# Kernel optimization log

Hardware: AMD Instinct MI355X
Metric: run time of the kernel (lower is better)

The kernel has to match this reference:

```python
import jax, jax.numpy as jnp
import numpy as np

BS, NQ, NTGT, NCLS, D = 16, 1024, 96, 4, 6
COST_CLASS, COST_BBOX = 1.0, 1.0
INF = jnp.float32(1e9)


def hungarian(cost):
    """Min-cost linear assignment (Jonker-Volgenant / e-maxx Hungarian).

    cost: (n, m) with n <= m. Returns (n,) int32: matched column for each row.
    Matches scipy.optimize.linear_sum_assignment's optimal assignment.
    """
    n, m = cost.shape
    # 1-indexed padded cost; row 0 / col 0 are virtual.
    a = jnp.zeros((n + 1, m + 1), jnp.float32).at[1:, 1:].set(cost.astype(jnp.float32))

    def assign_row(i, uvp):
        u, v, p = uvp  # p[j] = row matched to col j (0 = free)
        p = p.at[0].set(i)

        def dij_cond(c):
            _u, _v, _minv, _used, _way, j0 = c
            return p[j0] != 0

        def dij_body(c):
            u, v, minv, used, way, j0 = c
            used = used.at[j0].set(True)
            i0 = p[j0]
            cur = a[i0] - u[i0] - v                      # reduced costs, (m+1,)
            better = (cur < minv) & jnp.logical_not(used)
            minv = jnp.where(better, cur, minv)
            way = jnp.where(better, j0, way)
            masked = jnp.where(used, INF, minv)
            j1 = jnp.argmin(masked).astype(jnp.int32)
            delta = masked[j1]
            du = jnp.where(used, delta, jnp.float32(0))
            u = u.at[p].add(du)                          # u[p[j]] += delta for used j
            v = v - du
            minv = jnp.where(used, minv, minv - delta)
            return (u, v, minv, used, way, j1)

        minv0 = jnp.full(m + 1, INF, jnp.float32)
        used0 = jnp.zeros(m + 1, bool)
        way0 = jnp.zeros(m + 1, jnp.int32)
        u, v, _minv, _used, way, j0 = jax.lax.while_loop(
            dij_cond, dij_body, (u, v, minv0, used0, way0, jnp.int32(0)))

        def aug_cond(c):
            j0, _p = c
            return j0 != 0

        def aug_body(c):
            j0, p = c
            j1 = way[j0]
            p = p.at[j0].set(p[j1])
            return (j1, p)

        _, p = jax.lax.while_loop(aug_cond, aug_body, (j0, p))
        return (u, v, p)

    u0 = jnp.zeros(n + 1, jnp.float32)
    v0 = jnp.zeros(m + 1, jnp.float32)
    p0 = jnp.zeros(m + 1, jnp.int32)
    _, _, p = jax.lax.fori_loop(1, n + 1, assign_row, (u0, v0, p0))
    # invert: col4row[row] = col   (free cols / virtual col collapse into index 0)
    col4row = jnp.zeros(n + 1, jnp.int32).at[p[1:]].set(jnp.arange(1, m + 1, dtype=jnp.int32))
    return col4row[1:] - 1


def setup_inputs() -> dict:
    key = jax.random.key(0)
    k1, k2, k3, k4 = jax.random.split(key, 4)
    pred_logits = jax.random.normal(k1, (BS, NQ, NCLS), jnp.float32)
    pred_boxes = jax.random.uniform(k2, (BS, NQ, D), jnp.float32)
    labels = jax.random.randint(k3, (BS, NTGT), 0, NCLS, dtype=jnp.int32)
    control_points = jax.random.uniform(k4, (BS, NTGT, D), jnp.float32)
    return {"pred_logits": pred_logits, "pred_boxes": pred_boxes,
            "labels": labels, "control_points": control_points}


def reference(pred_logits, pred_boxes, labels, control_points):
    bs, nq, _ = pred_logits.shape
    ntgt = labels.shape[1]
    # cost matrix build (the memory-bound part)
    out_prob = jax.nn.softmax(pred_logits.reshape(bs * nq, -1), axis=-1)
    out_bbox = pred_boxes.reshape(bs * nq, -1)
    tgt_ids = labels.reshape(-1)
    tgt_bbox = control_points.reshape(bs * ntgt, -1)
    cost_class = -out_prob[:, tgt_ids]                              # (bs*nq, bs*ntgt)
    cost_bbox = jnp.abs(out_bbox[:, None, :] - tgt_bbox[None, :, :]).sum(-1)  # L1 cdist
    C = (COST_BBOX * cost_bbox + COST_CLASS * cost_class).reshape(bs, nq, bs * ntgt)

    # per-batch diagonal block -> Hungarian (targets as rows since ntgt <= nq)
    def per_batch(Cb, b):
        block = jax.lax.dynamic_slice(Cb, (0, b * ntgt), (nq, ntgt))  # (nq, ntgt)
        return hungarian(block.T)                                      # (ntgt,) matched query per target

    matched_query = jax.vmap(per_batch)(C, jnp.arange(bs, dtype=jnp.int32))
    return C, matched_query
```

## Files before the change

### kernel.cpp

```cpp
#include <hip/hip_runtime.h>


#define BSZ   16
#define NQ    1024
#define NTGT  96
#define NCLS  4
#define DD    6
#define NCOLS (BSZ * NTGT)
#define NROWS (BSZ * NQ)
#define LHINF 1e9f
#define NHB   16
#define ROWS_PER_BLK 8

typedef float f32x4 __attribute__((ext_vector_type(4)));

__device__ __forceinline__ float wave_fmin63(float x) {
    const int INF_I = __float_as_int(LHINF);
    int m;
    m = __builtin_amdgcn_update_dpp(INF_I, __float_as_int(x), 0x111, 0xf, 0xf, false);
    x = fminf(x, __int_as_float(m));
    m = __builtin_amdgcn_update_dpp(INF_I, __float_as_int(x), 0x112, 0xf, 0xf, false);
    x = fminf(x, __int_as_float(m));
    m = __builtin_amdgcn_update_dpp(INF_I, __float_as_int(x), 0x114, 0xf, 0xf, false);
    x = fminf(x, __int_as_float(m));
    m = __builtin_amdgcn_update_dpp(INF_I, __float_as_int(x), 0x118, 0xf, 0xf, false);
    x = fminf(x, __int_as_float(m));
    m = __builtin_amdgcn_update_dpp(INF_I, __float_as_int(x), 0x142, 0xf, 0xf, false);
    x = fminf(x, __int_as_float(m));
    m = __builtin_amdgcn_update_dpp(INF_I, __float_as_int(x), 0x143, 0xf, 0xf, false);
    x = fminf(x, __int_as_float(m));
    return x;
}

__device__ __forceinline__ float cost_elem6(const float* bx, const float* tv, float psel) {
    float cd = fabsf(bx[0] - tv[0]);
    cd += fabsf(bx[1] - tv[1]);
    cd += fabsf(bx[2] - tv[2]);
    cd += fabsf(bx[3] - tv[3]);
    cd += fabsf(bx[4] - tv[4]);
    cd += fabsf(bx[5] - tv[5]);
    return cd - psel;
}

__device__ __forceinline__ float4 softmax4(float4 lg) {
    const float mx = fmaxf(fmaxf(lg.x, lg.y), fmaxf(lg.z, lg.w));
    const float e0 = expf(lg.x - mx), e1 = expf(lg.y - mx);
    const float e2 = expf(lg.z - mx), e3 = expf(lg.w - mx);
    const float s = (e0 + e1) + (e2 + e3);
    return make_float4(e0 / s, e1 / s, e2 / s, e3 / s);
}

__global__ __launch_bounds__(256) void twsarg_kernel(
    const float* __restrict__ logits, const float* __restrict__ boxes,
    const int* __restrict__ labels, const float* __restrict__ tgt,
    float* __restrict__ tws, float* __restrict__ rowminv, int* __restrict__ rowarg)
{
    const int t = blockIdx.x;
    const int b = blockIdx.y;
    const int tr = b * NTGT + t;
    float tv[DD];
#pragma unroll
    for (int d = 0; d < DD; ++d) tv[d] = tgt[(size_t)tr * DD + d];
    const int cls = labels[tr];

    const int q4 = threadIdx.x * 4;
    const int row0 = b * NQ + q4;
    const float4* bx4 = (const float4*)(boxes + (size_t)row0 * DD);
    float bv[24];
#pragma unroll
    for (int c = 0; c < 6; ++c) {
        float4 f = bx4[c];
        bv[c * 4] = f.x; bv[c * 4 + 1] = f.y; bv[c * 4 + 2] = f.z; bv[c * 4 + 3] = f.w;
    }
    float o[4];
#pragma unroll
    for (int c = 0; c < 4; ++c) {
        const float4 p = softmax4(((const float4*)logits)[row0 + c]);
        const float ps = (cls == 0) ? p.x : (cls == 1) ? p.y : (cls == 2) ? p.z : p.w;
        o[c] = cost_elem6(bv + c * DD, tv, ps);
    }
    *((float4*)(tws + (size_t)tr * NQ + q4)) = make_float4(o[0], o[1], o[2], o[3]);

    float bvv = o[0]; int bj = q4;
    if (o[1] < bvv) { bvv = o[1]; bj = q4 + 1; }
    if (o[2] < bvv) { bvv = o[2]; bj = q4 + 2; }
    if (o[3] < bvv) { bvv = o[3]; bj = q4 + 3; }
#pragma unroll
    for (int off = 32; off > 0; off >>= 1) {
        const float ov = __shfl_down(bvv, off, 64);
        const int oj = __shfl_down(bj, off, 64);
        if (ov < bvv || (ov == bvv && oj < bj)) { bvv = ov; bj = oj; }
    }
    __shared__ float sv[4];
    __shared__ int sj[4];
    const int w = threadIdx.x >> 6;
    if ((threadIdx.x & 63) == 0) { sv[w] = bvv; sj[w] = bj; }
    __syncthreads();
    if (threadIdx.x == 0) {
        for (int i = 1; i < 4; ++i)
            if (sv[i] < bvv || (sv[i] == bvv && sj[i] < bj)) { bvv = sv[i]; bj = sj[i]; }
        rowminv[tr] = bvv; rowarg[tr] = bj;
    }
}

__global__ __launch_bounds__(384) void cost_kernel_fb(
    const float* __restrict__ logits, const float* __restrict__ boxes,
    const int* __restrict__ labels, const float* __restrict__ tgt,
    float* __restrict__ C)
{
    const int row = blockIdx.x;
    const int tid = threadIdx.x;
    const float4 pr = softmax4(*reinterpret_cast<const float4*>(logits + (size_t)row * NCLS));
    const float prr[4] = {pr.x, pr.y, pr.z, pr.w};
    float bx[DD];
#pragma unroll
    for (int d = 0; d < DD; ++d) bx[d] = boxes[(size_t)row * DD + d];
    const int colbase = tid * 4;
    const int4 lb = *reinterpret_cast<const int4*>(labels + colbase);
    const int cls[4] = {lb.x, lb.y, lb.z, lb.w};
    float tv[24];
    const float4* tg = reinterpret_cast<const float4*>(tgt + (size_t)colbase * DD);
#pragma unroll
    for (int d = 0; d < 6; ++d) {
        const float4 t4 = tg[d];
        tv[d * 4] = t4.x; tv[d * 4 + 1] = t4.y; tv[d * 4 + 2] = t4.z; tv[d * 4 + 3] = t4.w;
    }
    float o[4];
#pragma unroll
    for (int c = 0; c < 4; ++c) {
        const int cl = cls[c];
        const float ps = (cl == 0) ? prr[0] : (cl == 1) ? prr[1] : (cl == 2) ? prr[2] : prr[3];
        o[c] = cost_elem6(bx, tv + c * DD, ps);
    }
    *reinterpret_cast<float4*>(C + (size_t)row * NCOLS + colbase) =
        make_float4(o[0], o[1], o[2], o[3]);
}

__global__ __launch_bounds__(384) void fused_kernel(
    const float* __restrict__ tws, const float* __restrict__ logits,
    const float* __restrict__ boxes, const int* __restrict__ labels,
    const float* __restrict__ tgt,
    const float* __restrict__ rowminv, const int* __restrict__ rowarg,
    float* __restrict__ C, float* __restrict__ out_match, int warm)
{
    if (blockIdx.x >= NHB) {
        const int rb = (blockIdx.x - NHB) * ROWS_PER_BLK;
        const int tid = threadIdx.x;
        const int colbase = tid * 4;
        const int4 lb = ((const int4*)labels)[tid];
        const int cls[4] = {lb.x, lb.y, lb.z, lb.w};
        const float4* tg = (const float4*)(tgt + (size_t)colbase * DD);
        float tv[24];
#pragma unroll
        for (int c = 0; c < 6; ++c) {
            float4 f = tg[c];
            tv[c * 4] = f.x; tv[c * 4 + 1] = f.y; tv[c * 4 + 2] = f.z; tv[c * 4 + 3] = f.w;
        }
#pragma unroll
        for (int r = 0; r < ROWS_PER_BLK; ++r) {
            const int row = rb + r;
            const float4 pr = softmax4(((const float4*)logits)[row]);
            const float prr[4] = {pr.x, pr.y, pr.z, pr.w};
            const float* bp = boxes + (size_t)row * DD;
            float bx[DD];
#pragma unroll
            for (int d = 0; d < DD; ++d) bx[d] = bp[d];
            float o[4];
#pragma unroll
            for (int c = 0; c < 4; ++c) {
                const int cl = cls[c];
                const float ps = (cl == 0) ? prr[0] : (cl == 1) ? prr[1]
                               : (cl == 2) ? prr[2] : prr[3];
                o[c] = cost_elem6(bx, tv + c * DD, ps);
            }
            f32x4 ov;
            ov.x = o[0]; ov.y = o[1]; ov.z = o[2]; ov.w = o[3];
            __builtin_nontemporal_store(
                ov, (f32x4*)(C + (size_t)row * NCOLS + colbase));
        }
        return;
    }

    if (threadIdx.x >= 64) return;
    __builtin_amdgcn_s_setprio(2);
    const int b = blockIdx.x;
    const int lane = threadIdx.x;

    __shared__ float u_lds[NTGT + 1];
    __shared__ int   p_lds[NQ];
    __shared__ float dmark[NQ];
    __shared__ int   ja_s[NTGT];
    __shared__ float um_s[NTGT];
    __shared__ int   pendf[NTGT];

    for (int t = lane; t < NQ; t += 64) p_lds[t] = 0;
    for (int t = lane; t < NTGT + 1; t += 64) u_lds[t] = 0.f;
    __builtin_amdgcn_wave_barrier();

    const int jbase = lane * 16;
    const float* Tb = tws + (size_t)b * NTGT * NQ;
    const float* Cstr = C + (size_t)b * NQ * NCOLS + b * NTGT;

    float v[16], Msel[16], msk[16];
    int way[16], p_reg[16];
#pragma unroll
    for (int k = 0; k < 16; ++k) v[k] = 0.f;

    if (warm) {
        for (int t = lane; t < NTGT; t += 64) {
            ja_s[t] = rowarg[b * NTGT + t];
            um_s[t] = rowminv[b * NTGT + t];
        }
        __builtin_amdgcn_wave_barrier();
        if (lane == 0) {
            for (int t = 0; t < NTGT; ++t) {
                const int jt = ja_s[t];
                if (p_lds[jt] == 0) {
                    p_lds[jt] = t + 1;
                    u_lds[t + 1] = um_s[t];
                    pendf[t] = 0;
                } else {
                    pendf[t] = 1;
                }
            }
        }
        __builtin_amdgcn_wave_barrier();
    } else {
        for (int t = lane; t < NTGT; t += 64) pendf[t] = 1;
        __builtin_amdgcn_wave_barrier();
    }

    for (int tt = 0; tt < NTGT; ++tt) {
        const int pending = __builtin_amdgcn_readfirstlane(pendf[tt]);
        if (!pending) continue;
        const int i = tt + 1;

        const int4* pl4 = (const int4*)(p_lds + jbase);
#pragma unroll
        for (int c = 0; c < 4; ++c) {
            int4 pp = pl4[c];
            p_reg[c * 4] = pp.x; p_reg[c * 4 + 1] = pp.y;
            p_reg[c * 4 + 2] = pp.z; p_reg[c * 4 + 3] = pp.w;
        }
#pragma unroll
        for (int k = 0; k < 16; ++k) { Msel[k] = LHINF; msk[k] = -LHINF; way[k] = 0; }
        unsigned used = 0u;
        int i0 = i; float Delta = 0.f; int j0cur = 0;
        bool domark = false; int markk = 0;
        float Dfinal = 0.f; int jfreem1 = 0;

        for (;;) {
            float av[16];
            if (warm) {
                const float4* rp = (const float4*)(Tb + (size_t)(i0 - 1) * NQ + jbase);
#pragma unroll
                for (int c = 0; c < 4; ++c) {
                    float4 f = rp[c];
                    av[c * 4] = f.x; av[c * 4 + 1] = f.y;
                    av[c * 4 + 2] = f.z; av[c * 4 + 3] = f.w;
                }
            } else {
                const float* cp = Cstr + (i0 - 1);
#pragma unroll
                for (int k = 0; k < 16; ++k) av[k] = cp[(size_t)(jbase + k) * NCOLS];
            }
            const float u_i0 = u_lds[i0];

#pragma unroll
            for (int k = 0; k < 16; ++k) {
                const bool mk = domark && (markk == k);
                Msel[k] = mk ? LHINF : Msel[k];
                msk[k]  = mk ? LHINF : msk[k];
            }
            used |= (domark ? (1u << markk) : 0u);

            const float c0 = Delta - u_i0;
            float lbv = LHINF; int lbk = 0; int lbp = 0;
#pragma unroll
            for (int k = 0; k < 16; ++k) {
                float cand = (av[k] - v[k]) + c0;
                cand = fmaxf(cand, msk[k]);
                const bool better = cand < Msel[k];
                way[k]  = better ? j0cur : way[k];
                Msel[k] = better ? cand : Msel[k];
                const bool b2 = Msel[k] < lbv;
                lbv = b2 ? Msel[k] : lbv;
                lbk = b2 ? k : lbk;
                lbp = b2 ? p_reg[k] : lbp;
            }
            const float red = wave_fmin63(lbv);
            const float gmin = __int_as_float(
                __builtin_amdgcn_readlane(__float_as_int(red), 63));
            const unsigned long long bal = __ballot(lbv == gmin);
            const int W = __builtin_amdgcn_readfirstlane((int)__builtin_ctzll(bal));
            const int lbjm1 = jbase + lbk;
            const int j1m1 = __builtin_amdgcn_readlane(lbjm1, W);
            const int i0n  = __builtin_amdgcn_readlane(lbp, W);
            const bool iswin = (lane == W);
            if (iswin) dmark[lbjm1] = lbv;
            domark = iswin; markk = lbk;
            if (i0n == 0) { Dfinal = gmin; jfreem1 = j1m1; break; }
            Delta = gmin; i0 = i0n; j0cur = j1m1 + 1;
        }

        __builtin_amdgcn_wave_barrier();
        float dmv[16];
        const float4* dm4 = (const float4*)(dmark + jbase);
#pragma unroll
        for (int c = 0; c < 4; ++c) {
            float4 f = dm4[c];
            dmv[c * 4] = f.x; dmv[c * 4 + 1] = f.y;
            dmv[c * 4 + 2] = f.z; dmv[c * 4 + 3] = f.w;
        }
#pragma unroll
        for (int k = 0; k < 16; ++k) {
            if ((used >> k) & 1u) {
                const float d = Dfinal - dmv[k];
                v[k] -= d;
                u_lds[p_reg[k]] += d;
            }
        }
        if (lane == 0) u_lds[i] += Dfinal;
        __builtin_amdgcn_wave_barrier();

        int j0m1 = jfreem1;
        for (;;) {
            const int kk = j0m1 & 15;
            const int owner = __builtin_amdgcn_readfirstlane(j0m1 >> 4);
            int s0 = (kk & 1) ? way[1]  : way[0];
            int s1 = (kk & 1) ? way[3]  : way[2];
            int s2 = (kk & 1) ? way[5]  : way[4];
            int s3 = (kk & 1) ? way[7]  : way[6];
            int s4 = (kk & 1) ? way[9]  : way[8];
            int s5 = (kk & 1) ? way[11] : way[10];
            int s6 = (kk & 1) ? way[13] : way[12];
            int s7 = (kk & 1) ? way[15] : way[14];
            int t0 = (kk & 2) ? s1 : s0;
            int t1 = (kk & 2) ? s3 : s2;
            int t2 = (kk & 2) ? s5 : s4;
            int t3 = (kk & 2) ? s7 : s6;
            int q0 = (kk & 4) ? t1 : t0;
            int q1 = (kk & 4) ? t3 : t2;
            int wsel = (kk & 8) ? q1 : q0;
            const int jn = __builtin_amdgcn_readlane(wsel, owner);
            const int pv = (jn == 0) ? i : p_lds[jn - 1];
            if (lane == 0) p_lds[j0m1] = pv;
            __builtin_amdgcn_wave_barrier();
            if (jn == 0) break;
            j0m1 = jn - 1;
        }
    }

    for (int t = lane; t < NQ; t += 64) {
        const int r = p_lds[t];
        if (r > 0) out_match[b * NTGT + r - 1] = (float)t;
    }
}

extern "C" void kernel_launch(void* const* d_in, const int* in_sizes, int n_in,
                              void* d_out, int out_size, void* d_ws, size_t ws_size,
                              hipStream_t stream) {
    const float* logits = (const float*)d_in[0];
    const float* boxes  = (const float*)d_in[1];
    const int*   labels = (const int*)d_in[2];
    const float* tgt    = (const float*)d_in[3];

    float* C = (float*)d_out;
    float* out_match = C + (size_t)NROWS * NCOLS;

    const size_t tws_e = (size_t)NCOLS * NQ;
    const size_t rmv_e = (size_t)NCOLS;
    const size_t need = (tws_e + rmv_e * 2) * sizeof(float);

    if (d_ws != nullptr && ws_size >= need) {
        float* tws     = (float*)d_ws;
        float* rowminv = tws + tws_e;
        int*   rowarg  = (int*)(rowminv + rmv_e);
        twsarg_kernel<<<dim3(NTGT, BSZ), 256, 0, stream>>>(
            logits, boxes, labels, tgt, tws, rowminv, rowarg);
        fused_kernel<<<NHB + NROWS / ROWS_PER_BLK, 384, 0, stream>>>(
            tws, logits, boxes, labels, tgt, rowminv, rowarg, C, out_match, 1);
    } else {
        cost_kernel_fb<<<NROWS, 384, 0, stream>>>(logits, boxes, labels, tgt, C);
        fused_kernel<<<NHB, 64, 0, stream>>>(
            nullptr, logits, boxes, labels, tgt, nullptr, nullptr, C, out_match, 0);
    }
}
```

Before: 176.2 us.

## Prune Hungarian cost rows to top-K candidates staged in LDS

The candidate kernel no longer writes the full transposed cost rows. It bisects a threshold per target so that at least NTGT (and ideally at most KMAX) queries fall below it, then writes only those (value, column) pairs. The fused kernel loads every candidate for its batch into LDS once. In each Dijkstra step it scatters the current row's candidates into a dense INF-filled LDS row and clears them afterwards, replacing strided global reads with LDS accesses. This relies on the fact that an optimal match for a row lies among its n cheapest columns. The risks are ties pushing the count past KMAX, and a large static LDS footprint that may reduce occupancy of the cost-writing blocks in the same kernel.

```diff
diff --git a/kernel.cpp b/kernel.cpp
--- a/kernel.cpp
+++ b/kernel.cpp
@@ -9,8 +9,10 @@
 #define NCOLS (BSZ * NTGT)
 #define NROWS (BSZ * NQ)
 #define LHINF 1e9f
+#define FINITE_MAX 8.9e8f
 #define NHB   16
 #define ROWS_PER_BLK 8
+#define KMAX  112
 
 typedef float f32x4 __attribute__((ext_vector_type(4)));
 
@@ -50,10 +52,10 @@
     return make_float4(e0 / s, e1 / s, e2 / s, e3 / s);
 }
 
-__global__ __launch_bounds__(256) void twsarg_kernel(
+__global__ __launch_bounds__(256) void cand_kernel(
     const float* __restrict__ logits, const float* __restrict__ boxes,
     const int* __restrict__ labels, const float* __restrict__ tgt,
-    float* __restrict__ tws, float* __restrict__ rowminv, int* __restrict__ rowarg)
+    float2* __restrict__ cands, float* __restrict__ rowminv, int* __restrict__ rowarg)
 {
     const int t = blockIdx.x;
     const int b = blockIdx.y;
@@ -79,7 +81,6 @@
         const float ps = (cls == 0) ? p.x : (cls == 1) ? p.y : (cls == 2) ? p.z : p.w;
         o[c] = cost_elem6(bv + c * DD, tv, ps);
     }
-    *((float4*)(tws + (size_t)tr * NQ + q4)) = make_float4(o[0], o[1], o[2], o[3]);
 
     float bvv = o[0]; int bj = q4;
     if (o[1] < bvv) { bvv = o[1]; bj = q4 + 1; }
@@ -96,11 +97,51 @@
     const int w = threadIdx.x >> 6;
     if ((threadIdx.x & 63) == 0) { sv[w] = bvv; sj[w] = bj; }
     __syncthreads();
-    if (threadIdx.x == 0) {
-        for (int i = 1; i < 4; ++i)
-            if (sv[i] < bvv || (sv[i] == bvv && sj[i] < bj)) { bvv = sv[i]; bj = sj[i]; }
-        rowminv[tr] = bvv; rowarg[tr] = bj;
-    }
+    float rmin = sv[0]; int rarg = sj[0];
+#pragma unroll
+    for (int i = 1; i < 4; ++i)
+        if (sv[i] < rmin || (sv[i] == rmin && sj[i] < rarg)) { rmin = sv[i]; rarg = sj[i]; }
+
+    __shared__ int wcnt[2][4];
+    float lo = rmin, hi = rmin + 8.0f;
+    int cnt_hi = NQ;
+    for (int it = 0; it < 26; ++it) {
+        if (cnt_hi <= KMAX) break;
+        const float mid = 0.5f * (lo + hi);
+        const unsigned long long m0 = __ballot(o[0] < mid);
+        const unsigned long long m1 = __ballot(o[1] < mid);
+        const unsigned long long m2 = __ballot(o[2] < mid);
+        const unsigned long long m3 = __ballot(o[3] < mid);
+        if ((threadIdx.x & 63) == 0)
+            wcnt[it & 1][w] = (int)(__popcll(m0) + __popcll(m1) + __popcll(m2) + __popcll(m3));
+        __syncthreads();
+        const int c = wcnt[it & 1][0] + wcnt[it & 1][1] + wcnt[it & 1][2] + wcnt[it & 1][3];
+        if (c >= NTGT) { hi = mid; cnt_hi = c; } else { lo = mid; }
+    }
+    const float thr = hi;
+
+    __shared__ int pos;
+    __shared__ float cv_s[KMAX];
+    __shared__ int   cc_s[KMAX];
+    if (threadIdx.x == 0) pos = 0;
+    __syncthreads();
+#pragma unroll
+    for (int c = 0; c < 4; ++c) {
+        if (o[c] < thr) {
+            const int p = atomicAdd(&pos, 1);
+            if (p < KMAX) { cv_s[p] = o[c]; cc_s[p] = q4 + c; }
+        }
+    }
+    __syncthreads();
+    const int np = (pos < KMAX) ? pos : KMAX;
+    float2* out = cands + (size_t)tr * KMAX;
+    for (int i = threadIdx.x; i < KMAX; i += 256) {
+        float2 o2;
+        if (i < np) { o2.x = cv_s[i]; o2.y = __int_as_float(cc_s[i]); }
+        else        { o2.x = LHINF;   o2.y = __int_as_float(0); }
+        out[i] = o2;
+    }
+    if (threadIdx.x == 0) { rowminv[tr] = rmin; rowarg[tr] = rarg; }
 }
 
 __global__ __launch_bounds__(384) void cost_kernel_fb(
@@ -137,7 +178,7 @@
 }
 
 __global__ __launch_bounds__(384) void fused_kernel(
-    const float* __restrict__ tws, const float* __restrict__ logits,
+    const float2* __restrict__ cands, const float* __restrict__ logits,
     const float* __restrict__ boxes, const int* __restrict__ labels,
     const float* __restrict__ tgt,
     const float* __restrict__ rowminv, const int* __restrict__ rowarg,
@@ -181,11 +222,12 @@
         return;
     }
 
-    if (threadIdx.x >= 64) return;
-    __builtin_amdgcn_s_setprio(2);
     const int b = blockIdx.x;
-    const int lane = threadIdx.x;
-
+    const int tid = threadIdx.x;
+
+    __shared__ float cval_s[NTGT * KMAX];
+    __shared__ unsigned short ccol_s[NTGT * KMAX];
+    __shared__ float scat[NQ];
     __shared__ float u_lds[NTGT + 1];
     __shared__ int   p_lds[NQ];
     __shared__ float dmark[NQ];
@@ -193,12 +235,21 @@
     __shared__ float um_s[NTGT];
     __shared__ int   pendf[NTGT];
 
-    for (int t = lane; t < NQ; t += 64) p_lds[t] = 0;
-    for (int t = lane; t < NTGT + 1; t += 64) u_lds[t] = 0.f;
-    __builtin_amdgcn_wave_barrier();
+    if (warm) {
+        const float2* cg = cands + (size_t)b * NTGT * KMAX;
+        for (int i = tid; i < NTGT * KMAX; i += blockDim.x) {
+            const float2 cp = cg[i];
+            cval_s[i] = cp.x;
+            ccol_s[i] = (unsigned short)__float_as_int(cp.y);
+        }
+    }
+    for (int i = tid; i < NQ; i += blockDim.x) { scat[i] = LHINF; p_lds[i] = 0; }
+    for (int i = tid; i < NTGT + 1; i += blockDim.x) u_lds[i] = 0.f;
+    __syncthreads();
+    if (tid >= 64) return;
+    const int lane = tid;
 
     const int jbase = lane * 16;
-    const float* Tb = tws + (size_t)b * NTGT * NQ;
     const float* Cstr = C + (size_t)b * NQ * NCOLS + b * NTGT;
 
     float v[16], Msel[16], msk[16];
@@ -252,13 +303,28 @@
         for (;;) {
             float av[16];
             if (warm) {
-                const float4* rp = (const float4*)(Tb + (size_t)(i0 - 1) * NQ + jbase);
+                float cv0 = LHINF, cv1 = LHINF; int cc0 = 0, cc1 = 0;
+                if (lane < KMAX / 2) {
+                    const int cb = (i0 - 1) * KMAX + (lane << 1);
+                    cv0 = cval_s[cb];     cv1 = cval_s[cb + 1];
+                    cc0 = ccol_s[cb];     cc1 = ccol_s[cb + 1];
+                    if (cv0 < FINITE_MAX) scat[cc0] = cv0;
+                    if (cv1 < FINITE_MAX) scat[cc1] = cv1;
+                }
+                __builtin_amdgcn_wave_barrier();
+                const float4* sp = (const float4*)(scat + jbase);
 #pragma unroll
                 for (int c = 0; c < 4; ++c) {
-                    float4 f = rp[c];
+                    float4 f = sp[c];
                     av[c * 4] = f.x; av[c * 4 + 1] = f.y;
                     av[c * 4 + 2] = f.z; av[c * 4 + 3] = f.w;
                 }
+                __builtin_amdgcn_wave_barrier();
+                if (lane < KMAX / 2) {
+                    if (cv0 < FINITE_MAX) scat[cc0] = LHINF;
+                    if (cv1 < FINITE_MAX) scat[cc1] = LHINF;
+                }
+                __builtin_amdgcn_wave_barrier();
             } else {
                 const float* cp = Cstr + (i0 - 1);
 #pragma unroll
@@ -368,18 +434,18 @@
     float* C = (float*)d_out;
     float* out_match = C + (size_t)NROWS * NCOLS;
 
-    const size_t tws_e = (size_t)NCOLS * NQ;
-    const size_t rmv_e = (size_t)NCOLS;
-    const size_t need = (tws_e + rmv_e * 2) * sizeof(float);
+    const size_t cand_e = (size_t)NCOLS * KMAX;
+    const size_t rmv_e  = (size_t)NCOLS;
+    const size_t need = cand_e * sizeof(float2) + rmv_e * 2 * sizeof(float);
 
     if (d_ws != nullptr && ws_size >= need) {
-        float* tws     = (float*)d_ws;
-        float* rowminv = tws + tws_e;
-        int*   rowarg  = (int*)(rowminv + rmv_e);
-        twsarg_kernel<<<dim3(NTGT, BSZ), 256, 0, stream>>>(
-            logits, boxes, labels, tgt, tws, rowminv, rowarg);
+        float2* cands   = (float2*)d_ws;
+        float*  rowminv = (float*)(cands + cand_e);
+        int*    rowarg  = (int*)(rowminv + rmv_e);
+        cand_kernel<<<dim3(NTGT, BSZ), 256, 0, stream>>>(
+            logits, boxes, labels, tgt, cands, rowminv, rowarg);
         fused_kernel<<<NHB + NROWS / ROWS_PER_BLK, 384, 0, stream>>>(
-            tws, logits, boxes, labels, tgt, rowminv, rowarg, C, out_match, 1);
+            cands, logits, boxes, labels, tgt, rowminv, rowarg, C, out_match, 1);
     } else {
         cost_kernel_fb<<<NROWS, 384, 0, stream>>>(logits, boxes, labels, tgt, C);
         fused_kernel<<<NHB, 64, 0, stream>>>(
```

Result: slower. 185.0 us (+5.0%).
